# Kernel tuning notes

Hardware: AMD Instinct MI355X
Metric: run time of the kernel (lower is better)

Reference implementation:

```python
import jax, jax.numpy as jnp
import numpy as np

IN_CH = 256
OUT_CH = 128
N = 6144
ADJ_P = 0.01  # edge density -> avg degree ~61


def setup_inputs() -> dict:
    key = jax.random.key(0)
    ks = jax.random.split(key, 8)
    x = jax.random.normal(ks[0], (1, IN_CH, N), dtype=jnp.float32)
    adj = (jax.random.uniform(ks[1], (N, N)) < ADJ_P).astype(jnp.float32)
    W_fts = jax.random.normal(ks[2], (OUT_CH, IN_CH), dtype=jnp.float32) * 0.05
    w1 = jax.random.normal(ks[3], (OUT_CH,), dtype=jnp.float32) * 0.05
    b1 = jnp.zeros((1,), dtype=jnp.float32)
    w2 = jax.random.normal(ks[4], (OUT_CH,), dtype=jnp.float32) * 0.05
    b2 = jnp.zeros((1,), dtype=jnp.float32)
    vars_bias = jax.random.normal(ks[5], (1, N, OUT_CH), dtype=jnp.float32) * 0.02
    return {"x": x, "adj": adj, "W_fts": W_fts, "w1": w1, "b1": b1,
            "w2": w2, "b2": b2, "vars_bias": vars_bias}


def reference(x, adj, W_fts, w1, b1, w2, b2, vars_bias):
    # fts = Conv1d(in, out, k=1, bias=False)(x): [1, OUT_CH, N]
    fts = jnp.einsum('oi,bin->bon', W_fts, x)
    f = fts[0]  # [OUT_CH, N]
    # f1/f2 = Conv1d(out, 1, 1)(fts) -> per-node scalars [N]
    f1 = jnp.einsum('o,on->n', w1, f) + b1  # [N]
    f2 = jnp.einsum('o,on->n', w2, f) + b2  # [N]
    # scores[i,j] = leaky_relu(adj[i,j]*f1[i] + adj[i,j]*f2[j], 0.2)
    scores = jax.nn.leaky_relu(adj * f1[:, None] + adj * f2[None, :], 0.2)
    # sparse_softmax2d: per-row softmax masked to nonzero entries
    mask = (scores != 0).astype(scores.dtype)
    m = jnp.max(scores, axis=1, keepdims=True)  # stabilizer; cancels in ratio
    exps = jnp.exp(scores - m) * mask
    coefs = exps / jnp.sum(exps, axis=1, keepdims=True)  # [N, N]
    # vals = coefs @ fts.T : [N, OUT_CH]
    vals = coefs @ f.T
    # add bias, permute to [1, OUT_CH, N]
    ret = jnp.transpose(vals[None, :, :] + vars_bias, (0, 2, 1))
    return ret
```

## Files before the change

### kernel.cpp

```cpp
#include <hip/hip_runtime.h>

#define NN  6144
#define ICH 256
#define OCH 128
#define QW  160

typedef float vf4 __attribute__((ext_vector_type(4)));

__global__ __launch_bounds__(256) void k_fts(const float* __restrict__ x,
        const float* __restrict__ W, const float* __restrict__ w1,
        const float* __restrict__ w2, float* __restrict__ ft,
        float* __restrict__ f1, float* __restrict__ f2) {
    __shared__ float xs[32][32];
    __shared__ float Ws[32][OCH + 4];
    const int n0  = blockIdx.x * 32;
    const int tid = threadIdx.x;
    const int oq = (tid & 31) * 4;
    const int nq = (tid >> 5) * 4;
    float acc[4][4] = {};
    for (int k0 = 0; k0 < ICH; k0 += 32) {
        __syncthreads();
        {
            const int nn = tid & 31;
            const int kb = tid >> 5;
#pragma unroll
            for (int r = 0; r < 4; ++r)
                xs[kb + r * 8][nn] = x[(size_t)(k0 + kb + r * 8) * NN + n0 + nn];
        }
        {
            const int kk = tid & 31;
            const int ob = tid >> 5;
#pragma unroll
            for (int r = 0; r < 16; ++r) {
                const int o = ob + r * 8;
                Ws[kk][o] = W[o * ICH + k0 + kk];
            }
        }
        __syncthreads();
#pragma unroll
        for (int kk = 0; kk < 32; ++kk) {
            const float4 xv = *(const float4*)&xs[kk][nq];
            const float4 wv = *(const float4*)&Ws[kk][oq];
            const float xa[4] = {xv.x, xv.y, xv.z, xv.w};
            const float wa[4] = {wv.x, wv.y, wv.z, wv.w};
#pragma unroll
            for (int a = 0; a < 4; ++a)
#pragma unroll
                for (int b = 0; b < 4; ++b)
                    acc[a][b] = fmaf(xa[a], wa[b], acc[a][b]);
        }
    }
#pragma unroll
    for (int a = 0; a < 4; ++a) {
        float4 v = make_float4(acc[a][0], acc[a][1], acc[a][2], acc[a][3]);
        *(float4*)&ft[(size_t)(n0 + nq + a) * OCH + oq] = v;
    }
    const float4 w1v = *(const float4*)(w1 + oq);
    const float4 w2v = *(const float4*)(w2 + oq);
    float p1[4], p2[4];
#pragma unroll
    for (int a = 0; a < 4; ++a) {
        p1[a] = acc[a][0] * w1v.x + acc[a][1] * w1v.y + acc[a][2] * w1v.z + acc[a][3] * w1v.w;
        p2[a] = acc[a][0] * w2v.x + acc[a][1] * w2v.y + acc[a][2] * w2v.z + acc[a][3] * w2v.w;
    }
#pragma unroll
    for (int m = 16; m > 0; m >>= 1) {
#pragma unroll
        for (int a = 0; a < 4; ++a) {
            p1[a] += __shfl_xor(p1[a], m);
            p2[a] += __shfl_xor(p2[a], m);
        }
    }
    if ((tid & 31) == 0) {
#pragma unroll
        for (int a = 0; a < 4; ++a) {
            f1[n0 + nq + a] = p1[a];
            f2[n0 + nq + a] = p2[a];
        }
    }
}

__global__ __launch_bounds__(256) void k_attn(const float* __restrict__ adj,
        const float* __restrict__ ft, const float* __restrict__ f1,
        const float* __restrict__ f2, const float* __restrict__ b1,
        const float* __restrict__ b2, const float* __restrict__ vb,
        float* __restrict__ out) {
    __shared__ float q_e[4][QW];
    __shared__ int   q_j[4][QW];
    __shared__ int   qc[4];
    const int tid  = threadIdx.x;
    const int lane = tid & 63;
    const int wave = tid >> 6;
    const int i = (blockIdx.x & 7) * 768 + (blockIdx.x >> 3) * 4 + wave;
    if (lane == 0) qc[wave] = 0;
    const float s1 = f1[i] + b1[0] + b2[0];
    const float* arow = adj + (size_t)i * NN;
    float den = 0.f;
    vf4 ab[2][6];
#pragma unroll
    for (int w = 0; w < 6; ++w)
        ab[0][w] = __builtin_nontemporal_load((const vf4*)(arow + lane * 4 + w * 256));
#pragma unroll
    for (int b = 0; b < 4; ++b) {
        if (b < 3) {
#pragma unroll
            for (int w = 0; w < 6; ++w)
                ab[(b + 1) & 1][w] = __builtin_nontemporal_load(
                    (const vf4*)(arow + (b + 1) * 1536 + lane * 4 + w * 256));
        }
#pragma unroll
        for (int w = 0; w < 6; ++w) {
            const vf4 a4 = ab[b & 1][w];
            const int j0 = b * 1536 + w * 256 + lane * 4;
            const int k = (a4.x != 0.f) + (a4.y != 0.f) + (a4.z != 0.f) + (a4.w != 0.f);
            if (k) {
                const float4 g = *(const float4*)(f2 + j0);
                int slot = atomicAdd(&qc[wave], k);
                if (slot + k <= QW) {
                    if (a4.x != 0.f) { float s = s1 + g.x; s = s > 0.f ? s : 0.2f * s;
                                       float e = __expf(s); den += e;
                                       q_j[wave][slot] = j0;     q_e[wave][slot] = e; ++slot; }
                    if (a4.y != 0.f) { float s = s1 + g.y; s = s > 0.f ? s : 0.2f * s;
                                       float e = __expf(s); den += e;
                                       q_j[wave][slot] = j0 + 1; q_e[wave][slot] = e; ++slot; }
                    if (a4.z != 0.f) { float s = s1 + g.z; s = s > 0.f ? s : 0.2f * s;
                                       float e = __expf(s); den += e;
                                       q_j[wave][slot] = j0 + 2; q_e[wave][slot] = e; ++slot; }
                    if (a4.w != 0.f) { float s = s1 + g.w; s = s > 0.f ? s : 0.2f * s;
                                       float e = __expf(s); den += e;
                                       q_j[wave][slot] = j0 + 3; q_e[wave][slot] = e; }
                }
            }
        }
    }
#pragma unroll
    for (int off = 32; off > 0; off >>= 1) den += __shfl_xor(den, off);
    const float inv = 1.f / den;
    const int nE = qc[wave] < QW ? qc[wave] : QW;
    const int half = lane >> 5;
    const int c0 = (lane & 31) * 4;
    float4 nm = make_float4(0.f, 0.f, 0.f, 0.f);
#pragma unroll 2
    for (int idx = half; idx < nE; idx += 2) {
        const int   j = q_j[wave][idx];
        const float e = q_e[wave][idx];
        const float4 g = *(const float4*)(ft + (size_t)j * OCH + c0);
        nm.x = fmaf(e, g.x, nm.x);
        nm.y = fmaf(e, g.y, nm.y);
        nm.z = fmaf(e, g.z, nm.z);
        nm.w = fmaf(e, g.w, nm.w);
    }
    nm.x += __shfl_xor(nm.x, 32);
    nm.y += __shfl_xor(nm.y, 32);
    nm.z += __shfl_xor(nm.z, 32);
    nm.w += __shfl_xor(nm.w, 32);
    if (half == 0) {
        const float4 bv = *(const float4*)(vb + (size_t)i * OCH + c0);
        out[(size_t)(c0    ) * NN + i] = fmaf(nm.x, inv, bv.x);
        out[(size_t)(c0 + 1) * NN + i] = fmaf(nm.y, inv, bv.y);
        out[(size_t)(c0 + 2) * NN + i] = fmaf(nm.z, inv, bv.z);
        out[(size_t)(c0 + 3) * NN + i] = fmaf(nm.w, inv, bv.w);
    }
}

extern "C" void kernel_launch(void* const* d_in, const int* in_sizes, int n_in,
                              void* d_out, int out_size, void* d_ws, size_t ws_size,
                              hipStream_t stream) {
    const float* x   = (const float*)d_in[0];
    const float* adj = (const float*)d_in[1];
    const float* W   = (const float*)d_in[2];
    const float* w1  = (const float*)d_in[3];
    const float* b1  = (const float*)d_in[4];
    const float* w2  = (const float*)d_in[5];
    const float* b2  = (const float*)d_in[6];
    const float* vb  = (const float*)d_in[7];
    float* out = (float*)d_out;

    char* ws = (char*)d_ws;
    float* ft = (float*)ws;
    float* f1 = (float*)(ws + 3145728);
    float* f2 = (float*)(ws + 3145728 + 24576);

    k_fts<<<dim3(NN / 32), 256, 0, stream>>>(x, W, w1, w2, ft, f1, f2);
    k_attn<<<dim3(NN / 4), 256, 0, stream>>>(adj, ft, f1, f2, b1, b2, vb, out);
}
```

Baseline: 259.7 us.

## Split adjacency scan into bitmask compaction, then wave-parallel exp with prefix-sum placement

```diff
diff --git a/kernel.cpp b/kernel.cpp
--- a/kernel.cpp
+++ b/kernel.cpp
@@ -84,9 +84,10 @@
         const float* __restrict__ ft, const float* __restrict__ f1,
         const float* __restrict__ f2, const float* __restrict__ b1,
         const float* __restrict__ b2, const float* __restrict__ vb,
-        float* __restrict__ out) {
-    __shared__ float q_e[4][QW];
-    __shared__ int   q_j[4][QW];
+        float* __restrict__ vals) {
+    __shared__ int   qw[4][QW];
+    __shared__ int   eq_j[4][QW];
+    __shared__ float eq_e[4][QW];
     __shared__ int   qc[4];
     const int tid  = threadIdx.x;
     const int lane = tid & 63;
@@ -95,7 +96,6 @@
     if (lane == 0) qc[wave] = 0;
     const float s1 = f1[i] + b1[0] + b2[0];
     const float* arow = adj + (size_t)i * NN;
-    float den = 0.f;
     vf4 ab[2][6];
 #pragma unroll
     for (int w = 0; w < 6; ++w)
@@ -112,38 +112,57 @@
         for (int w = 0; w < 6; ++w) {
             const vf4 a4 = ab[b & 1][w];
             const int j0 = b * 1536 + w * 256 + lane * 4;
-            const int k = (a4.x != 0.f) + (a4.y != 0.f) + (a4.z != 0.f) + (a4.w != 0.f);
-            if (k) {
-                const float4 g = *(const float4*)(f2 + j0);
-                int slot = atomicAdd(&qc[wave], k);
-                if (slot + k <= QW) {
-                    if (a4.x != 0.f) { float s = s1 + g.x; s = s > 0.f ? s : 0.2f * s;
-                                       float e = __expf(s); den += e;
-                                       q_j[wave][slot] = j0;     q_e[wave][slot] = e; ++slot; }
-                    if (a4.y != 0.f) { float s = s1 + g.y; s = s > 0.f ? s : 0.2f * s;
-                                       float e = __expf(s); den += e;
-                                       q_j[wave][slot] = j0 + 1; q_e[wave][slot] = e; ++slot; }
-                    if (a4.z != 0.f) { float s = s1 + g.z; s = s > 0.f ? s : 0.2f * s;
-                                       float e = __expf(s); den += e;
-                                       q_j[wave][slot] = j0 + 2; q_e[wave][slot] = e; ++slot; }
-                    if (a4.w != 0.f) { float s = s1 + g.w; s = s > 0.f ? s : 0.2f * s;
-                                       float e = __expf(s); den += e;
-                                       q_j[wave][slot] = j0 + 3; q_e[wave][slot] = e; }
-                }
+            const int m = (a4.x != 0.f ? 1 : 0) | (a4.y != 0.f ? 2 : 0)
+                        | (a4.z != 0.f ? 4 : 0) | (a4.w != 0.f ? 8 : 0);
+            if (m) {
+                const int slot = atomicAdd(&qc[wave], 1);
+                if (slot < QW) qw[wave][slot] = (j0 << 4) | m;
             }
+        }
+    }
+    const int nW = qc[wave] < QW ? qc[wave] : QW;
+    float den = 0.f;
+    int off0 = 0;
+    for (int t0 = 0; t0 < nW; t0 += 64) {
+        const int t = t0 + lane;
+        int jb = 0, mm = 0, kc = 0;
+        float e0 = 0.f, e1 = 0.f, e2 = 0.f, e3 = 0.f;
+        if (t < nW) {
+            const int entry = qw[wave][t];
+            jb = entry >> 4; mm = entry & 15;
+            kc = __popc(mm);
+            const float4 g = *(const float4*)(f2 + jb);
+            if (mm & 1) { float s = s1 + g.x; s = s > 0.f ? s : 0.2f * s; e0 = __expf(s); den += e0; }
+            if (mm & 2) { float s = s1 + g.y; s = s > 0.f ? s : 0.2f * s; e1 = __expf(s); den += e1; }
+            if (mm & 4) { float s = s1 + g.z; s = s > 0.f ? s : 0.2f * s; e2 = __expf(s); den += e2; }
+            if (mm & 8) { float s = s1 + g.w; s = s > 0.f ? s : 0.2f * s; e3 = __expf(s); den += e3; }
+        }
+        int pf = kc;
+#pragma unroll
+        for (int off = 1; off < 64; off <<= 1) {
+            const int y = __shfl_up(pf, off);
+            if (lane >= off) pf += y;
+        }
+        int slot = off0 + pf - kc;
+        off0 += __shfl(pf, 63);
+        if (t < nW) {
+            if (mm & 1) { if (slot < QW) { eq_j[wave][slot] = jb;     eq_e[wave][slot] = e0; } ++slot; }
+            if (mm & 2) { if (slot < QW) { eq_j[wave][slot] = jb + 1; eq_e[wave][slot] = e1; } ++slot; }
+            if (mm & 4) { if (slot < QW) { eq_j[wave][slot] = jb + 2; eq_e[wave][slot] = e2; } ++slot; }
+            if (mm & 8) { if (slot < QW) { eq_j[wave][slot] = jb + 3; eq_e[wave][slot] = e3; } ++slot; }
         }
     }
 #pragma unroll
     for (int off = 32; off > 0; off >>= 1) den += __shfl_xor(den, off);
     const float inv = 1.f / den;
-    const int nE = qc[wave] < QW ? qc[wave] : QW;
+    const int nE = off0 < QW ? off0 : QW;
     const int half = lane >> 5;
     const int c0 = (lane & 31) * 4;
     float4 nm = make_float4(0.f, 0.f, 0.f, 0.f);
-#pragma unroll 2
+#pragma unroll 4
     for (int idx = half; idx < nE; idx += 2) {
-        const int   j = q_j[wave][idx];
-        const float e = q_e[wave][idx];
+        const int   j = eq_j[wave][idx];
+        const float e = eq_e[wave][idx];
         const float4 g = *(const float4*)(ft + (size_t)j * OCH + c0);
         nm.x = fmaf(e, g.x, nm.x);
         nm.y = fmaf(e, g.y, nm.y);
@@ -156,11 +175,27 @@
     nm.w += __shfl_xor(nm.w, 32);
     if (half == 0) {
         const float4 bv = *(const float4*)(vb + (size_t)i * OCH + c0);
-        out[(size_t)(c0    ) * NN + i] = fmaf(nm.x, inv, bv.x);
-        out[(size_t)(c0 + 1) * NN + i] = fmaf(nm.y, inv, bv.y);
-        out[(size_t)(c0 + 2) * NN + i] = fmaf(nm.z, inv, bv.z);
-        out[(size_t)(c0 + 3) * NN + i] = fmaf(nm.w, inv, bv.w);
-    }
+        float4 r;
+        r.x = fmaf(nm.x, inv, bv.x);
+        r.y = fmaf(nm.y, inv, bv.y);
+        r.z = fmaf(nm.z, inv, bv.z);
+        r.w = fmaf(nm.w, inv, bv.w);
+        *(float4*)&vals[(size_t)i * OCH + c0] = r;
+    }
+}
+
+__global__ __launch_bounds__(256) void k_tr(const float* __restrict__ v,
+                                            float* __restrict__ out) {
+    __shared__ float t[32][33];
+    const int i0 = blockIdx.x * 32;
+    const int c0 = blockIdx.y * 32;
+    const int r = threadIdx.x >> 3;
+    const int q = (threadIdx.x & 7) * 4;
+    const float4 a = *(const float4*)&v[(size_t)(i0 + r) * OCH + c0 + q];
+    t[r][q] = a.x; t[r][q + 1] = a.y; t[r][q + 2] = a.z; t[r][q + 3] = a.w;
+    __syncthreads();
+    const float4 o = make_float4(t[q][r], t[q + 1][r], t[q + 2][r], t[q + 3][r]);
+    *(float4*)&out[(size_t)(c0 + r) * NN + i0 + q] = o;
 }
 
 extern "C" void kernel_launch(void* const* d_in, const int* in_sizes, int n_in,
@@ -177,10 +212,12 @@
     float* out = (float*)d_out;
 
     char* ws = (char*)d_ws;
-    float* ft = (float*)ws;
-    float* f1 = (float*)(ws + 3145728);
-    float* f2 = (float*)(ws + 3145728 + 24576);
+    float* ft   = (float*)ws;
+    float* f1   = (float*)(ws + 3145728);
+    float* f2   = (float*)(ws + 3145728 + 24576);
+    float* vals = (float*)(ws + 3145728 + 49152);
 
     k_fts<<<dim3(NN / 32), 256, 0, stream>>>(x, W, w1, w2, ft, f1, f2);
-    k_attn<<<dim3(NN / 4), 256, 0, stream>>>(adj, ft, f1, f2, b1, b2, vb, out);
-}
+    k_attn<<<dim3(NN / 4), 256, 0, stream>>>(adj, ft, f1, f2, b1, b2, vb, vals);
+    k_tr<<<dim3(NN / 32, OCH / 32), 256, 0, stream>>>(vals, out);
+}
```

Result: no change. 256.2 us (-1.4%).
